# Optimization experiments

Hardware: AMD Instinct MI355X
Metric: run time of the kernel (lower is better)

## Reference

```python
import jax, jax.numpy as jnp
import numpy as np

B, T, C = 2, 2048, 768
H = 12
HD = C // H  # 64
DFF = 4 * C
EPS = 1e-5


def setup_inputs() -> dict:
    key = jax.random.key(0)
    ks = jax.random.split(key, 12)
    s = 0.02
    return {
        "x": jax.random.normal(ks[0], (B, T, C), dtype=jnp.float32),
        "ln1_g": jnp.ones((C,), jnp.float32),
        "ln1_b": jnp.zeros((C,), jnp.float32),
        "w_qkv": jax.random.normal(ks[1], (C, 3 * C), dtype=jnp.float32) * s,
        "w_o": jax.random.normal(ks[2], (C, C), dtype=jnp.float32) * s,
        "ln2_g": jnp.ones((C,), jnp.float32),
        "ln2_b": jnp.zeros((C,), jnp.float32),
        "w_fc": jax.random.normal(ks[3], (C, DFF), dtype=jnp.float32) * s,
        "b_fc": jnp.zeros((DFF,), jnp.float32),
        "w_proj": jax.random.normal(ks[4], (DFF, C), dtype=jnp.float32) * s,
        "b_proj": jnp.zeros((C,), jnp.float32),
    }


def _layernorm(x, g, b):
    mu = jnp.mean(x, axis=-1, keepdims=True)
    var = jnp.mean(jnp.square(x - mu), axis=-1, keepdims=True)
    return (x - mu) * jax.lax.rsqrt(var + EPS) * g + b


def _attn(x, w_qkv, w_o):
    b, t, c = x.shape
    qkv = x @ w_qkv  # [b,t,3c]
    q, k, v = jnp.split(qkv, 3, axis=-1)
    q = q.reshape(b, t, H, HD).transpose(0, 2, 1, 3)  # [b,h,t,d]
    k = k.reshape(b, t, H, HD).transpose(0, 2, 1, 3)
    v = v.reshape(b, t, H, HD).transpose(0, 2, 1, 3)
    att = jnp.einsum("bhqd,bhkd->bhqk", q, k) / jnp.sqrt(jnp.float32(HD))
    causal = jnp.tril(jnp.ones((t, t), dtype=bool))
    att = jnp.where(causal, att, -jnp.inf)
    att = jax.nn.softmax(att, axis=-1)
    y = jnp.einsum("bhqk,bhkd->bhqd", att, v)
    y = y.transpose(0, 2, 1, 3).reshape(b, t, c)
    return y @ w_o


def reference(x, ln1_g, ln1_b, w_qkv, w_o, ln2_g, ln2_b, w_fc, b_fc, w_proj, b_proj):
    x = x + _attn(_layernorm(x, ln1_g, ln1_b), w_qkv, w_o)
    h = _layernorm(x, ln2_g, ln2_b)
    h = jax.nn.gelu(h @ w_fc + b_fc, approximate=False)  # torch F.gelu default = exact erf
    x = x + (h @ w_proj + b_proj)
    return x
```

## Files before the change

kernel.cpp:

```cpp
#include <hip/hip_runtime.h>
#include <hip/hip_bf16.h>
#include <math.h>

#define T_SEQ 2048
#define NB 2
#define C_DIM 768
#define NH 12

typedef unsigned short ushort_t;
typedef __attribute__((ext_vector_type(8))) short short8;
typedef __attribute__((ext_vector_type(8))) unsigned short ushort8;
typedef __attribute__((ext_vector_type(4))) unsigned short ushortx4;
typedef __attribute__((ext_vector_type(4))) float floatx4;
typedef __attribute__((ext_vector_type(4))) _Float16 half4;

__device__ inline float bf2f(ushort_t u) {
    unsigned int x = ((unsigned int)u) << 16;
    return __uint_as_float(x);
}
__device__ inline ushort_t f2bf(float f) {
    unsigned int u = __float_as_uint(f);
    unsigned int r = (u + 0x7fffu + ((u >> 16) & 1u)) >> 16;
    return (ushort_t)r;
}
__device__ inline ushort_t f2h_bits(float f) {
    union { _Float16 h; ushort_t u; } cv;
    cv.h = (_Float16)f;
    return cv.u;
}

#if defined(__has_builtin)
#if __has_builtin(__builtin_amdgcn_global_load_lds)
#define HAVE_GLL 1
#endif
#endif

__device__ inline void gload_lds16(const ushort_t* g, ushort_t* l) {
#ifdef HAVE_GLL
    __builtin_amdgcn_global_load_lds(
        (const __attribute__((address_space(1))) void*)g,
        (__attribute__((address_space(3))) void*)l, 16, 0, 0);
#else
    int lane = threadIdx.x & 63;
    *(ushort8*)(l + lane * 8) = *(const ushort8*)g;
#endif
}

__device__ void wconv_tile(const float* __restrict__ W, ushort_t* __restrict__ WT,
                           int K, int N, int k0, int n0, int tid, ushort_t* Tls) {
    int nl = (tid & 15) * 4;
    int kl = tid >> 4;
#pragma unroll
    for (int rr = 0; rr < 4; rr++) {
        int k = kl + rr * 16;
        floatx4 v = *(const floatx4*)&W[(size_t)(k0 + k) * N + n0 + nl];
#pragma unroll
        for (int j = 0; j < 4; j++) Tls[(nl + j) * 72 + k] = f2bf(v[j]);
    }
    __syncthreads();
    int no = tid >> 3;
    int ko = (tid & 7) * 8;
#pragma unroll
    for (int rr = 0; rr < 2; rr++) {
        int n = no + rr * 32;
        ushort8 t = *(const ushort8*)&Tls[n * 72 + ko];
        *(ushort8*)&WT[(size_t)(n0 + n) * K + k0 + ko] = t;
    }
}

__global__ __launch_bounds__(256) void prep1_kernel(const float* __restrict__ w_qkv, ushort_t* __restrict__ wqkvT,
                                                    const float* __restrict__ w_o, ushort_t* __restrict__ woT,
                                                    const float* __restrict__ w_fc, ushort_t* __restrict__ wfcT,
                                                    const float* __restrict__ w_proj, ushort_t* __restrict__ wprojT,
                                                    const float* __restrict__ x, const float* __restrict__ g,
                                                    const float* __restrict__ b, ushort_t* __restrict__ xn) {
    __shared__ ushort_t Tls[64 * 72];
    __shared__ float red[8];
    int id = blockIdx.x, tid = threadIdx.x;
    if (id < 432) { wconv_tile(w_qkv, wqkvT, 768, 2304, (id % 12) * 64, (id / 12) * 64, tid, Tls); return; }
    if (id < 576) { int r = id - 432; wconv_tile(w_o, woT, 768, 768, (r % 12) * 64, (r / 12) * 64, tid, Tls); return; }
    if (id < 1152) { int r = id - 576; wconv_tile(w_fc, wfcT, 768, 3072, (r % 12) * 64, (r / 12) * 64, tid, Tls); return; }
    if (id < 1728) { int r = id - 1152; wconv_tile(w_proj, wprojT, 3072, 768, (r % 48) * 64, (r / 48) * 64, tid, Tls); return; }
    int row = id - 1728;
    int lane = tid & 63, wave = tid >> 6;
    const float* xr = x + (size_t)row * C_DIM;
    float v0 = xr[tid], v1 = xr[tid + 256], v2 = xr[tid + 512];
    float s = v0 + v1 + v2;
#pragma unroll
    for (int m = 32; m > 0; m >>= 1) s += __shfl_xor(s, m, 64);
    if (lane == 0) red[wave] = s;
    __syncthreads();
    float mean = (red[0] + red[1] + red[2] + red[3]) * (1.0f / C_DIM);
    float d0 = v0 - mean, d1 = v1 - mean, d2 = v2 - mean;
    float q = d0 * d0 + d1 * d1 + d2 * d2;
#pragma unroll
    for (int m = 32; m > 0; m >>= 1) q += __shfl_xor(q, m, 64);
    if (lane == 0) red[wave + 4] = q;
    __syncthreads();
    float var = (red[4] + red[5] + red[6] + red[7]) * (1.0f / C_DIM);
    float rstd = rsqrtf(var + 1e-5f);
    ushort_t* orow = xn + (size_t)row * C_DIM;
    orow[tid]       = f2bf(d0 * rstd * g[tid]       + b[tid]);
    orow[tid + 256] = f2bf(d1 * rstd * g[tid + 256] + b[tid + 256]);
    orow[tid + 512] = f2bf(d2 * rstd * g[tid + 512] + b[tid + 512]);
}

__global__ __launch_bounds__(192) void combine_ln_kernel(const float* __restrict__ x,
                                                         const ushort_t* __restrict__ P,
                                                         const float* __restrict__ g,
                                                         const float* __restrict__ bb,
                                                         float* __restrict__ x2,
                                                         ushort_t* __restrict__ xn) {
    int row = blockIdx.x;
    int tid = threadIdx.x;
    int lane = tid & 63, wave = tid >> 6;
    int col = tid * 4;
    size_t idx = (size_t)row * C_DIM + col;
    floatx4 xv = *(const floatx4*)&x[idx];
    ushortx4 a = *(const ushortx4*)&P[idx];
    ushortx4 b2 = *(const ushortx4*)&P[3145728 + idx];
    ushortx4 c2 = *(const ushortx4*)&P[6291456 + idx];
    floatx4 v;
#pragma unroll
    for (int j = 0; j < 4; j++) v[j] = xv[j] + bf2f(a[j]) + bf2f(b2[j]) + bf2f(c2[j]);
    *(floatx4*)&x2[idx] = v;

    float s = v[0] + v[1] + v[2] + v[3];
#pragma unroll
    for (int m = 32; m > 0; m >>= 1) s += __shfl_xor(s, m, 64);
    __shared__ float red[6];
    if (lane == 0) red[wave] = s;
    __syncthreads();
    float mean = (red[0] + red[1] + red[2]) * (1.0f / C_DIM);
    floatx4 d;
#pragma unroll
    for (int j = 0; j < 4; j++) d[j] = v[j] - mean;
    float q = d[0] * d[0] + d[1] * d[1] + d[2] * d[2] + d[3] * d[3];
#pragma unroll
    for (int m = 32; m > 0; m >>= 1) q += __shfl_xor(q, m, 64);
    if (lane == 0) red[wave + 3] = q;
    __syncthreads();
    float var = (red[3] + red[4] + red[5]) * (1.0f / C_DIM);
    float rstd = rsqrtf(var + 1e-5f);
    floatx4 gv = *(const floatx4*)&g[col];
    floatx4 bv = *(const floatx4*)&bb[col];
    ushortx4 o;
#pragma unroll
    for (int j = 0; j < 4; j++) o[j] = f2bf(d[j] * rstd * gv[j] + bv[j]);
    *(ushortx4*)&xn[idx] = o;
}

#define GEMM_LOOP(Aptr, Bptr, KDIM, KLEN, KOFF)                                        \
    __shared__ ushort_t As[128 * 64];                                                  \
    __shared__ ushort_t Bs[128 * 64];                                                  \
    int tid = threadIdx.x;                                                             \
    int lane = tid & 63, wave = tid >> 6;                                              \
    int lane15 = lane & 15, quad = lane >> 4;                                          \
    int wr = wave >> 1, wc = wave & 1;                                                 \
    int row0 = blockIdx.x * 128, col0 = blockIdx.y * 128;                              \
    int srow = lane >> 3;                                                              \
    int sseg = (lane & 7) ^ srow;                                                      \
    const ushort_t* ag[4]; const ushort_t* bg[4];                                      \
    ushort_t* la[4]; ushort_t* lb[4];                                                  \
    _Pragma("unroll")                                                                  \
    for (int j = 0; j < 4; j++) {                                                      \
        int r = wave * 32 + j * 8;                                                     \
        ag[j] = Aptr + (size_t)(row0 + r + srow) * KDIM + KOFF + sseg * 8;             \
        bg[j] = Bptr + (size_t)(col0 + r + srow) * KDIM + KOFF + sseg * 8;             \
        la[j] = &As[r * 64]; lb[j] = &Bs[r * 64];                                      \
    }                                                                                  \
    floatx4 acc[4][4];                                                                 \
    floatx4 zero = {0.f, 0.f, 0.f, 0.f};                                               \
    _Pragma("unroll")                                                                  \
    for (int mt = 0; mt < 4; mt++)                                                     \
        _Pragma("unroll")                                                              \
        for (int nt = 0; nt < 4; nt++) acc[mt][nt] = zero;                             \
    for (int k0 = 0; k0 < KLEN; k0 += 64) {                                            \
        _Pragma("unroll")                                                              \
        for (int j = 0; j < 4; j++) gload_lds16(ag[j] + k0, la[j]);                    \
        _Pragma("unroll")                                                              \
        for (int j = 0; j < 4; j++) gload_lds16(bg[j] + k0, lb[j]);                    \
        __syncthreads();                                                               \
        _Pragma("unroll")                                                              \
        for (int ko = 0; ko < 2; ko++) {                                               \
            int slot = (quad + ko * 4) ^ (lane15 & 7);                                 \
            short8 af[4], bfm[4];                                                      \
            _Pragma("unroll")                                                          \
            for (int mt = 0; mt < 4; mt++)                                             \
                af[mt] = *(const short8*)&As[(wr * 64 + mt * 16 + lane15) * 64 + slot * 8]; \
            _Pragma("unroll")                                                          \
            for (int nt = 0; nt < 4; nt++)                                             \
                bfm[nt] = *(const short8*)&Bs[(wc * 64 + nt * 16 + lane15) * 64 + slot * 8]; \
            _Pragma("unroll")                                                          \
            for (int mt = 0; mt < 4; mt++)                                             \
                _Pragma("unroll")                                                      \
                for (int nt = 0; nt < 4; nt++)                                         \
                    acc[mt][nt] = __builtin_amdgcn_mfma_f32_16x16x32_bf16(af[mt], bfm[nt], acc[mt][nt], 0, 0, 0); \
        }                                                                              \
        __syncthreads();                                                               \
    }

__global__ __launch_bounds__(256) void gemm_qkv_kernel(const ushort_t* __restrict__ A,
                                                       const ushort_t* __restrict__ BT,
                                                       ushort_t* __restrict__ qbuf,
                                                       ushort_t* __restrict__ kh,
                                                       ushort_t* __restrict__ vtb) {
    GEMM_LOOP(A, BT, 768, 768, 0)
    int yb = blockIdx.y;
    if (yb < 6) {
#pragma unroll
        for (int mt = 0; mt < 4; mt++) {
            int r_base = row0 + wr * 64 + mt * 16 + quad * 4;
#pragma unroll
            for (int nt = 0; nt < 4; nt++) {
                int cc = col0 + wc * 64 + nt * 16 + lane15;
#pragma unroll
                for (int r = 0; r < 4; r++)
                    qbuf[(size_t)(r_base + r) * 768 + cc] = f2bf(acc[mt][nt][r]);
            }
        }
    } else if (yb < 12) {
#pragma unroll
        for (int mt = 0; mt < 4; mt++) {
            int r_base = row0 + wr * 64 + mt * 16 + quad * 4;
#pragma unroll
            for (int nt = 0; nt < 4; nt++) {
                int colk = col0 - 768 + wc * 64 + nt * 16 + lane15;
                int hh = colk >> 6, dd = colk & 63;
#pragma unroll
                for (int r = 0; r < 4; r++) {
                    int rr = r_base + r;
                    kh[((size_t)((rr >> 11) * NH + hh)) * 131072 + (size_t)(rr & 2047) * 64 + dd] =
                        f2bf(acc[mt][nt][r]);
                }
            }
        }
    } else {
#pragma unroll
        for (int mt = 0; mt < 4; mt++) {
            int r_base = row0 + wr * 64 + mt * 16 + quad * 4;
            int bb2 = r_base >> 11;
            int tt = r_base & 2047;
#pragma unroll
            for (int nt = 0; nt < 4; nt++) {
                int colv = col0 - 1536 + wc * 64 + nt * 16 + lane15;
                int hh = colv >> 6, dd = colv & 63;
                size_t va = ((size_t)(bb2 * NH + hh)) * 131072 + (size_t)(tt >> 4) * 1024 +
                            (size_t)dd * 16 + (tt & 15);
                ushortx4 pv;
#pragma unroll
                for (int r = 0; r < 4; r++) pv[r] = f2h_bits(acc[mt][nt][r]);
                *(ushortx4*)&vtb[va] = pv;
            }
        }
    }
}

__global__ __launch_bounds__(256) void gemm_gelu_kernel(const ushort_t* __restrict__ A,
                                                        const ushort_t* __restrict__ BT,
                                                        const float* __restrict__ bias,
                                                        ushort_t* __restrict__ Cout) {
    GEMM_LOOP(A, BT, 768, 768, 0)
    const int N = 3072;
#pragma unroll
    for (int mt = 0; mt < 4; mt++) {
        int r_base = row0 + wr * 64 + mt * 16 + quad * 4;
#pragma unroll
        for (int nt = 0; nt < 4; nt++) {
            int cc = col0 + wc * 64 + nt * 16 + lane15;
            float bvv = bias[cc];
#pragma unroll
            for (int r = 0; r < 4; r++) {
                float v = acc[mt][nt][r] + bvv;
                float y2 = v * (2.3022079f + 0.10294323f * v * v);
                float e = __builtin_amdgcn_exp2f(-y2);
                v = v * __builtin_amdgcn_rcpf(1.f + e);
                Cout[(size_t)(r_base + r) * N + cc] = f2bf(v);
            }
        }
    }
}

__global__ __launch_bounds__(256) void gemm_bt_split_kernel(const ushort_t* __restrict__ A,
                                                            const ushort_t* __restrict__ BT,
                                                            ushort_t* __restrict__ P,
                                                            int M, int N, int K, int klen) {
    int kz0 = blockIdx.z * klen;
    GEMM_LOOP(A, BT, K, klen, kz0)
    ushort_t* Pz = P + (size_t)blockIdx.z * M * N;
#pragma unroll
    for (int mt = 0; mt < 4; mt++) {
        int r_base = row0 + wr * 64 + mt * 16 + quad * 4;
#pragma unroll
        for (int nt = 0; nt < 4; nt++) {
            int cc = col0 + wc * 64 + nt * 16 + lane15;
#pragma unroll
            for (int r = 0; r < 4; r++)
                Pz[(size_t)(r_base + r) * N + cc] = f2bf(acc[mt][nt][r]);
        }
    }
}

__global__ __launch_bounds__(256) void combine_bias_res_kernel(float* __restrict__ x2,
                                                               const float* __restrict__ bias,
                                                               const ushort_t* __restrict__ P) {
    int i = blockIdx.x * 256 + threadIdx.x;
    int col = (i * 4) % C_DIM;
    floatx4 xv = *(const floatx4*)&x2[i * 4];
    floatx4 bv = *(const floatx4*)&bias[col];
    ushortx4 a = *(const ushortx4*)&P[i * 4];
    ushortx4 b = *(const ushortx4*)&P[3145728 + i * 4];
    floatx4 o;
#pragma unroll
    for (int j = 0; j < 4; j++) o[j] = xv[j] + bv[j] + bf2f(a[j]) + bf2f(b[j]);
    *(floatx4*)&x2[i * 4] = o;
}

#define QSCALE 0.18033688f
__global__ __launch_bounds__(256) void attn_kernel(const ushort_t* __restrict__ qbuf,
                                                   const ushort_t* __restrict__ kh,
                                                   const ushort_t* __restrict__ vtb,
                                                   ushort_t* __restrict__ y) {
    __shared__ ushort_t Kb[2][4096];
    __shared__ ushort_t Vb[2][4096];
    int tid = threadIdx.x;
    int lane = tid & 63, wave = tid >> 6;
    int lane15 = lane & 15, quad = lane >> 4;
    int qt = 31 - (int)blockIdx.x;
    int q0 = qt * 64;
    int h = blockIdx.y, b = blockIdx.z;
    size_t hb = (size_t)(b * NH + h) * (T_SEQ * 64);
    const ushort_t* khb = kh + hb;
    const ushort_t* vtbb = vtb + hb;

    int q = q0 + wave * 16 + lane15;
    int qmax_wave = q0 + wave * 16 + 15;
    short8 qf[2];
#pragma unroll
    for (int c = 0; c < 2; c++) {
        ushort8 qv = *(const ushort8*)(qbuf + ((size_t)b * T_SEQ + q) * 768 + h * 64 + c * 32 + quad * 8);
        short8 qs;
#pragma unroll
        for (int j = 0; j < 8; j++) qs[j] = (short)f2bf(bf2f(qv[j]) * QSCALE);
        qf[c] = qs;
    }

    floatx4 o[4];
    floatx4 zero = {0.f, 0.f, 0.f, 0.f};
#pragma unroll
    for (int nt = 0; nt < 4; nt++) o[nt] = zero;
    float l4[4] = {0.f, 0.f, 0.f, 0.f};

    int tiles = qt + 1;
    int vsrc = lane ^ ((lane >> 3) & 1);

    {
        if (wave < 2) {
#pragma unroll
            for (int j = 0; j < 4; j++) {
                int r = wave * 4 + j;
                int i = r * 64 + lane;
                int key = i >> 3;
                int seg = ((i & 7) - (key & 7) + 8) & 7;
                gload_lds16(khb + (size_t)key * 64 + seg * 8, &Kb[0][(size_t)r * 512]);
            }
        } else {
#pragma unroll
            for (int j = 0; j < 4; j++) {
                int r = (wave - 2) * 4 + j;
                gload_lds16(vtbb + (size_t)r * 512 + vsrc * 8, &Vb[0][(size_t)r * 512]);
            }
        }
    }

    for (int t = 0; t < tiles; t++) {
        int kb = t * 64;
        int cur = t & 1;
        __syncthreads();
        if (t + 1 < tiles) {
            int kb2 = kb + 64;
            int nxt = cur ^ 1;
            if (wave < 2) {
#pragma unroll
                for (int j = 0; j < 4; j++) {
                    int r = wave * 4 + j;
                    int i = r * 64 + lane;
                    int key = i >> 3;
                    int seg = ((i & 7) - (key & 7) + 8) & 7;
                    gload_lds16(khb + (size_t)(kb2 + key) * 64 + seg * 8, &Kb[nxt][(size_t)r * 512]);
                }
            } else {
#pragma unroll
                for (int j = 0; j < 4; j++) {
                    int r = (wave - 2) * 4 + j;
                    gload_lds16(vtbb + (size_t)(kb2 >> 4) * 1024 + (size_t)r * 512 + vsrc * 8,
                                &Vb[nxt][(size_t)r * 512]);
                }
            }
        }

        if (kb <= qmax_wave) {
            const ushort_t* Kc = Kb[cur];
            const _Float16* Vc = (const _Float16*)Vb[cur];

            floatx4 s[4];
#pragma unroll
            for (int sb = 0; sb < 4; sb++) {
                int key = sb * 16 + lane15;
                int s0i = key * 8 + ((quad + key) & 7);
                int s1i = key * 8 + ((quad + 4 + key) & 7);
                short8 kf0 = *(const short8*)(Kc + (size_t)s0i * 8);
                short8 kf1 = *(const short8*)(Kc + (size_t)s1i * 8);
                floatx4 sv = zero;
                sv = __builtin_amdgcn_mfma_f32_16x16x32_bf16(kf0, qf[0], sv, 0, 0, 0);
                sv = __builtin_amdgcn_mfma_f32_16x16x32_bf16(kf1, qf[1], sv, 0, 0, 0);
                s[sb] = sv;
            }

            if (kb + 64 > qmax_wave) {
#pragma unroll
                for (int sb = 0; sb < 4; sb++)
#pragma unroll
                    for (int r = 0; r < 4; r++) {
                        int key = kb + sb * 16 + quad * 4 + r;
                        if (key > q) s[sb][r] = -INFINITY;
                    }
            }

            half4 pf[4];
#pragma unroll
            for (int sb = 0; sb < 4; sb++)
#pragma unroll
                for (int r = 0; r < 4; r++) {
                    float p = __builtin_amdgcn_exp2f(s[sb][r]);
                    l4[r] += p;
                    pf[sb][r] = (_Float16)p;
                }

#pragma unroll
            for (int sb = 0; sb < 4; sb++) {
#pragma unroll
                for (int nt = 0; nt < 4; nt++) {
                    int gg = sb * 128 + (nt * 16 + lane15) * 2 + (quad >> 1);
                    int ss = gg ^ ((gg >> 3) & 1);
                    half4 vf = *(const half4*)&Vc[(size_t)ss * 8 + (quad & 1) * 4];
                    o[nt] = __builtin_amdgcn_mfma_f32_16x16x16f16(vf, pf[sb], o[nt], 0, 0, 0);
                }
            }
        }
    }

    float l_i = (l4[0] + l4[1]) + (l4[2] + l4[3]);
    l_i += __shfl_xor(l_i, 16, 64);
    l_i += __shfl_xor(l_i, 32, 64);
    float rcp_w = 1.f / l_i;
    ushort_t* yb = y + (size_t)b * T_SEQ * 768;
#pragma unroll
    for (int nt = 0; nt < 4; nt++) {
        ushortx4 st;
#pragma unroll
        for (int r = 0; r < 4; r++) st[r] = f2bf(o[nt][r] * rcp_w);
        *(ushortx4*)&yb[(size_t)q * 768 + h * 64 + nt * 16 + quad * 4] = st;
    }
}

extern "C" void kernel_launch(void* const* d_in, const int* in_sizes, int n_in,
                              void* d_out, int out_size, void* d_ws, size_t ws_size,
                              hipStream_t stream) {
    (void)in_sizes; (void)n_in; (void)out_size; (void)ws_size;
    const float* x      = (const float*)d_in[0];
    const float* ln1_g  = (const float*)d_in[1];
    const float* ln1_b  = (const float*)d_in[2];
    const float* w_qkv  = (const float*)d_in[3];
    const float* w_o    = (const float*)d_in[4];
    const float* ln2_g  = (const float*)d_in[5];
    const float* ln2_b  = (const float*)d_in[6];
    const float* w_fc   = (const float*)d_in[7];
    const float* b_fc   = (const float*)d_in[8];
    const float* w_proj = (const float*)d_in[9];
    const float* b_proj = (const float*)d_in[10];

    char* ws = (char*)d_ws;
    ushort_t* qbuf   = (ushort_t*)(ws);
    ushort_t* kh     = (ushort_t*)(ws + 6291456);
    ushort_t* vtb    = (ushort_t*)(ws + 12582912);
    ushort_t* PA     = (ushort_t*)(ws);
    ushort_t* hff    = (ushort_t*)(ws);
    ushort_t* ybuf   = (ushort_t*)(ws + 18874368);
    ushort_t* xn     = (ushort_t*)(ws + 25165824);
    ushort_t* PB     = (ushort_t*)(ws + 25165824);
    ushort_t* wqkvT  = (ushort_t*)(ws + 31457280);
    ushort_t* woT    = (ushort_t*)(ws + 34996224);
    ushort_t* wfcT   = (ushort_t*)(ws + 36175872);
    ushort_t* wprojT = (ushort_t*)(ws + 40894464);
    float* x2 = (float*)d_out;

    const int M = NB * T_SEQ;

    prep1_kernel<<<dim3(5824), 256, 0, stream>>>(w_qkv, wqkvT, w_o, woT, w_fc, wfcT,
                                                 w_proj, wprojT, x, ln1_g, ln1_b, xn);
    gemm_qkv_kernel<<<dim3(32, 18), 256, 0, stream>>>(xn, wqkvT, qbuf, kh, vtb);
    attn_kernel<<<dim3(32, 12, 2), 256, 0, stream>>>(qbuf, kh, vtb, ybuf);
    gemm_bt_split_kernel<<<dim3(32, 6, 3), 256, 0, stream>>>(ybuf, woT, PA, M, 768, 768, 256);
    combine_ln_kernel<<<dim3(M), 192, 0, stream>>>(x, PA, ln2_g, ln2_b, x2, xn);
    gemm_gelu_kernel<<<dim3(32, 24), 256, 0, stream>>>(xn, wfcT, b_fc, hff);
    gemm_bt_split_kernel<<<dim3(32, 6, 2), 256, 0, stream>>>(hff, wprojT, PB, M, 768, 3072, 1536);
    combine_bias_res_kernel<<<dim3(3072), 256, 0, stream>>>(x2, b_proj, PB);
}
```

Before: 265.9 us.

## Process two 16-row query groups per wave in attention to reuse K/V tiles

Each attention block now covers 128 queries instead of 64, with each wave handling two 16-query groups that share the same K and V fragments loaded from LDS. This halves the grid and the number of K/V tile loads per query, cutting global and LDS traffic per unit of work. The cost is more registers per thread (double accumulators and scores), which may lower occupancy. There are also fewer blocks (384), so load balance across the causal triangle gets coarser.

```diff
diff --git a/kernel.cpp b/kernel.cpp
--- a/kernel.cpp
+++ b/kernel.cpp
@@ -326,32 +326,41 @@
     int tid = threadIdx.x;
     int lane = tid & 63, wave = tid >> 6;
     int lane15 = lane & 15, quad = lane >> 4;
-    int qt = 31 - (int)blockIdx.x;
-    int q0 = qt * 64;
+    int qt = 15 - (int)blockIdx.x;
+    int q0 = qt * 128;
     int h = blockIdx.y, b = blockIdx.z;
     size_t hb = (size_t)(b * NH + h) * (T_SEQ * 64);
     const ushort_t* khb = kh + hb;
     const ushort_t* vtbb = vtb + hb;
 
-    int q = q0 + wave * 16 + lane15;
-    int qmax_wave = q0 + wave * 16 + 15;
-    short8 qf[2];
-#pragma unroll
-    for (int c = 0; c < 2; c++) {
-        ushort8 qv = *(const ushort8*)(qbuf + ((size_t)b * T_SEQ + q) * 768 + h * 64 + c * 32 + quad * 8);
-        short8 qs;
-#pragma unroll
-        for (int j = 0; j < 8; j++) qs[j] = (short)f2bf(bf2f(qv[j]) * QSCALE);
-        qf[c] = qs;
-    }
-
-    floatx4 o[4];
+    int qA = q0 + wave * 32 + lane15;
+    int qB = qA + 16;
+    int qmaxA = q0 + wave * 32 + 15;
+    int qmaxB = qmaxA + 16;
+
+    short8 qf[2][2];
+#pragma unroll
+    for (int g = 0; g < 2; g++) {
+        int qq = (g == 0) ? qA : qB;
+#pragma unroll
+        for (int c = 0; c < 2; c++) {
+            ushort8 qv = *(const ushort8*)(qbuf + ((size_t)b * T_SEQ + qq) * 768 + h * 64 + c * 32 + quad * 8);
+            short8 qs;
+#pragma unroll
+            for (int j = 0; j < 8; j++) qs[j] = (short)f2bf(bf2f(qv[j]) * QSCALE);
+            qf[g][c] = qs;
+        }
+    }
+
+    floatx4 o[2][4];
     floatx4 zero = {0.f, 0.f, 0.f, 0.f};
 #pragma unroll
-    for (int nt = 0; nt < 4; nt++) o[nt] = zero;
-    float l4[4] = {0.f, 0.f, 0.f, 0.f};
-
-    int tiles = qt + 1;
+    for (int g = 0; g < 2; g++)
+#pragma unroll
+        for (int nt = 0; nt < 4; nt++) o[g][nt] = zero;
+    float l4[2][4] = {{0.f, 0.f, 0.f, 0.f}, {0.f, 0.f, 0.f, 0.f}};
+
+    int tiles = qt * 2 + 2;
     int vsrc = lane ^ ((lane >> 3) & 1);
 
     {
@@ -399,11 +408,12 @@
             }
         }
 
-        if (kb <= qmax_wave) {
+        if (kb <= qmaxB) {
             const ushort_t* Kc = Kb[cur];
             const _Float16* Vc = (const _Float16*)Vb[cur];
-
-            floatx4 s[4];
+            bool doA = (kb <= qmaxA);
+
+            floatx4 sA[4], sB[4];
 #pragma unroll
             for (int sb = 0; sb < 4; sb++) {
                 int key = sb * 16 + lane15;
@@ -412,30 +422,55 @@
                 short8 kf0 = *(const short8*)(Kc + (size_t)s0i * 8);
                 short8 kf1 = *(const short8*)(Kc + (size_t)s1i * 8);
                 floatx4 sv = zero;
-                sv = __builtin_amdgcn_mfma_f32_16x16x32_bf16(kf0, qf[0], sv, 0, 0, 0);
-                sv = __builtin_amdgcn_mfma_f32_16x16x32_bf16(kf1, qf[1], sv, 0, 0, 0);
-                s[sb] = sv;
-            }
-
-            if (kb + 64 > qmax_wave) {
+                sv = __builtin_amdgcn_mfma_f32_16x16x32_bf16(kf0, qf[1][0], sv, 0, 0, 0);
+                sv = __builtin_amdgcn_mfma_f32_16x16x32_bf16(kf1, qf[1][1], sv, 0, 0, 0);
+                sB[sb] = sv;
+                if (doA) {
+                    floatx4 sv2 = zero;
+                    sv2 = __builtin_amdgcn_mfma_f32_16x16x32_bf16(kf0, qf[0][0], sv2, 0, 0, 0);
+                    sv2 = __builtin_amdgcn_mfma_f32_16x16x32_bf16(kf1, qf[0][1], sv2, 0, 0, 0);
+                    sA[sb] = sv2;
+                }
+            }
+
+            if (kb + 64 > qmaxB) {
 #pragma unroll
                 for (int sb = 0; sb < 4; sb++)
 #pragma unroll
                     for (int r = 0; r < 4; r++) {
                         int key = kb + sb * 16 + quad * 4 + r;
-                        if (key > q) s[sb][r] = -INFINITY;
+                        if (key > qB) sB[sb][r] = -INFINITY;
                     }
             }
-
-            half4 pf[4];
+            if (doA && kb + 64 > qmaxA) {
+#pragma unroll
+                for (int sb = 0; sb < 4; sb++)
+#pragma unroll
+                    for (int r = 0; r < 4; r++) {
+                        int key = kb + sb * 16 + quad * 4 + r;
+                        if (key > qA) sA[sb][r] = -INFINITY;
+                    }
+            }
+
+            half4 pfA[4], pfB[4];
 #pragma unroll
             for (int sb = 0; sb < 4; sb++)
 #pragma unroll
                 for (int r = 0; r < 4; r++) {
-                    float p = __builtin_amdgcn_exp2f(s[sb][r]);
-                    l4[r] += p;
-                    pf[sb][r] = (_Float16)p;
+                    float p = __builtin_amdgcn_exp2f(sB[sb][r]);
+                    l4[1][r] += p;
+                    pfB[sb][r] = (_Float16)p;
                 }
+            if (doA) {
+#pragma unroll
+                for (int sb = 0; sb < 4; sb++)
+#pragma unroll
+                    for (int r = 0; r < 4; r++) {
+                        float p = __builtin_amdgcn_exp2f(sA[sb][r]);
+                        l4[0][r] += p;
+                        pfA[sb][r] = (_Float16)p;
+                    }
+            }
 
 #pragma unroll
             for (int sb = 0; sb < 4; sb++) {
@@ -444,23 +479,29 @@
                     int gg = sb * 128 + (nt * 16 + lane15) * 2 + (quad >> 1);
                     int ss = gg ^ ((gg >> 3) & 1);
                     half4 vf = *(const half4*)&Vc[(size_t)ss * 8 + (quad & 1) * 4];
-                    o[nt] = __builtin_amdgcn_mfma_f32_16x16x16f16(vf, pf[sb], o[nt], 0, 0, 0);
+                    o[1][nt] = __builtin_amdgcn_mfma_f32_16x16x16f16(vf, pfB[sb], o[1][nt], 0, 0, 0);
+                    if (doA)
+                        o[0][nt] = __builtin_amdgcn_mfma_f32_16x16x16f16(vf, pfA[sb], o[0][nt], 0, 0, 0);
                 }
             }
         }
     }
 
-    float l_i = (l4[0] + l4[1]) + (l4[2] + l4[3]);
-    l_i += __shfl_xor(l_i, 16, 64);
-    l_i += __shfl_xor(l_i, 32, 64);
-    float rcp_w = 1.f / l_i;
     ushort_t* yb = y + (size_t)b * T_SEQ * 768;
 #pragma unroll
-    for (int nt = 0; nt < 4; nt++) {
-        ushortx4 st;
-#pragma unroll
-        for (int r = 0; r < 4; r++) st[r] = f2bf(o[nt][r] * rcp_w);
-        *(ushortx4*)&yb[(size_t)q * 768 + h * 64 + nt * 16 + quad * 4] = st;
+    for (int g = 0; g < 2; g++) {
+        float l_i = (l4[g][0] + l4[g][1]) + (l4[g][2] + l4[g][3]);
+        l_i += __shfl_xor(l_i, 16, 64);
+        l_i += __shfl_xor(l_i, 32, 64);
+        float rcp_w = 1.f / l_i;
+        int qq = (g == 0) ? qA : qB;
+#pragma unroll
+        for (int nt = 0; nt < 4; nt++) {
+            ushortx4 st;
+#pragma unroll
+            for (int r = 0; r < 4; r++) st[r] = f2bf(o[g][nt][r] * rcp_w);
+            *(ushortx4*)&yb[(size_t)qq * 768 + h * 64 + nt * 16 + quad * 4] = st;
+        }
     }
 }
 
@@ -500,7 +541,7 @@
     prep1_kernel<<<dim3(5824), 256, 0, stream>>>(w_qkv, wqkvT, w_o, woT, w_fc, wfcT,
                                                  w_proj, wprojT, x, ln1_g, ln1_b, xn);
     gemm_qkv_kernel<<<dim3(32, 18), 256, 0, stream>>>(xn, wqkvT, qbuf, kh, vtb);
-    attn_kernel<<<dim3(32, 12, 2), 256, 0, stream>>>(qbuf, kh, vtb, ybuf);
+    attn_kernel<<<dim3(16, 12, 2), 256, 0, stream>>>(qbuf, kh, vtb, ybuf);
     gemm_bt_split_kernel<<<dim3(32, 6, 3), 256, 0, stream>>>(ybuf, woT, PA, M, 768, 768, 256);
     combine_ln_kernel<<<dim3(M), 192, 0, stream>>>(x, PA, ln2_g, ln2_b, x2, xn);
     gemm_gelu_kernel<<<dim3(32, 24), 256, 0, stream>>>(xn, wfcT, b_fc, hff);
```

Measured after the change: 286.1 us. 7.6% more time.

## Split long causal attention tiles across two blocks and combine partial outputs

Applied to the files above, without the earlier changes.

The upper half of query tiles, which have the most key tiles under causal masking, are now each split into two blocks that process disjoint halves of the key range. Each half writes unnormalized fp16 partial outputs and row sums to workspace, and a new combine kernel sums them and normalizes. The aim is better load balance and more blocks to fill the GPU during attention. The cost is an extra launch, extra global traffic for the partials, and fp16 storage of the unnormalized accumulators. The combine drops any max-subtraction and simply adds both halves' sums, which is only correct if the kernel does not track a running max, as the original code appears not to.

```diff
diff --git a/kernel.cpp b/kernel.cpp
--- a/kernel.cpp
+++ b/kernel.cpp
@@ -320,15 +320,32 @@
 __global__ __launch_bounds__(256) void attn_kernel(const ushort_t* __restrict__ qbuf,
                                                    const ushort_t* __restrict__ kh,
                                                    const ushort_t* __restrict__ vtb,
-                                                   ushort_t* __restrict__ y) {
+                                                   ushort_t* __restrict__ y,
+                                                   ushort_t* __restrict__ OP,
+                                                   float* __restrict__ LP) {
     __shared__ ushort_t Kb[2][4096];
     __shared__ ushort_t Vb[2][4096];
     int tid = threadIdx.x;
     int lane = tid & 63, wave = tid >> 6;
     int lane15 = lane & 15, quad = lane >> 4;
-    int qt = 31 - (int)blockIdx.x;
+    int c = blockIdx.x;
+    int h = blockIdx.y, b = blockIdx.z;
+    int qt, t_start, t_end, half = 0;
+    bool is_half;
+    if (c < 32) {
+        qt = 16 + (c >> 1);
+        half = c & 1;
+        int ntl = qt + 1, mid = ntl >> 1;
+        t_start = half ? mid : 0;
+        t_end = half ? ntl : mid;
+        is_half = true;
+    } else {
+        qt = c - 32;
+        t_start = 0;
+        t_end = qt + 1;
+        is_half = false;
+    }
     int q0 = qt * 64;
-    int h = blockIdx.y, b = blockIdx.z;
     size_t hb = (size_t)(b * NH + h) * (T_SEQ * 64);
     const ushort_t* khb = kh + hb;
     const ushort_t* vtbb = vtb + hb;
@@ -337,12 +354,12 @@
     int qmax_wave = q0 + wave * 16 + 15;
     short8 qf[2];
 #pragma unroll
-    for (int c = 0; c < 2; c++) {
-        ushort8 qv = *(const ushort8*)(qbuf + ((size_t)b * T_SEQ + q) * 768 + h * 64 + c * 32 + quad * 8);
+    for (int cc2 = 0; cc2 < 2; cc2++) {
+        ushort8 qv = *(const ushort8*)(qbuf + ((size_t)b * T_SEQ + q) * 768 + h * 64 + cc2 * 32 + quad * 8);
         short8 qs;
 #pragma unroll
         for (int j = 0; j < 8; j++) qs[j] = (short)f2bf(bf2f(qv[j]) * QSCALE);
-        qf[c] = qs;
+        qf[cc2] = qs;
     }
 
     floatx4 o[4];
@@ -351,10 +368,11 @@
     for (int nt = 0; nt < 4; nt++) o[nt] = zero;
     float l4[4] = {0.f, 0.f, 0.f, 0.f};
 
-    int tiles = qt + 1;
     int vsrc = lane ^ ((lane >> 3) & 1);
 
     {
+        int kb = t_start * 64;
+        int buf = t_start & 1;
         if (wave < 2) {
 #pragma unroll
             for (int j = 0; j < 4; j++) {
@@ -362,22 +380,23 @@
                 int i = r * 64 + lane;
                 int key = i >> 3;
                 int seg = ((i & 7) - (key & 7) + 8) & 7;
-                gload_lds16(khb + (size_t)key * 64 + seg * 8, &Kb[0][(size_t)r * 512]);
+                gload_lds16(khb + (size_t)(kb + key) * 64 + seg * 8, &Kb[buf][(size_t)r * 512]);
             }
         } else {
 #pragma unroll
             for (int j = 0; j < 4; j++) {
                 int r = (wave - 2) * 4 + j;
-                gload_lds16(vtbb + (size_t)r * 512 + vsrc * 8, &Vb[0][(size_t)r * 512]);
-            }
-        }
-    }
-
-    for (int t = 0; t < tiles; t++) {
+                gload_lds16(vtbb + (size_t)(kb >> 4) * 1024 + (size_t)r * 512 + vsrc * 8,
+                            &Vb[buf][(size_t)r * 512]);
+            }
+        }
+    }
+
+    for (int t = t_start; t < t_end; t++) {
         int kb = t * 64;
         int cur = t & 1;
         __syncthreads();
-        if (t + 1 < tiles) {
+        if (t + 1 < t_end) {
             int kb2 = kb + 64;
             int nxt = cur ^ 1;
             if (wave < 2) {
@@ -453,14 +472,49 @@
     float l_i = (l4[0] + l4[1]) + (l4[2] + l4[3]);
     l_i += __shfl_xor(l_i, 16, 64);
     l_i += __shfl_xor(l_i, 32, 64);
-    float rcp_w = 1.f / l_i;
-    ushort_t* yb = y + (size_t)b * T_SEQ * 768;
-#pragma unroll
-    for (int nt = 0; nt < 4; nt++) {
-        ushortx4 st;
-#pragma unroll
-        for (int r = 0; r < 4; r++) st[r] = f2bf(o[nt][r] * rcp_w);
-        *(ushortx4*)&yb[(size_t)q * 768 + h * 64 + nt * 16 + quad * 4] = st;
+
+    if (!is_half) {
+        float rcp_w = 1.f / l_i;
+        ushort_t* yb = y + (size_t)b * T_SEQ * 768;
+#pragma unroll
+        for (int nt = 0; nt < 4; nt++) {
+            ushortx4 st;
+#pragma unroll
+            for (int r = 0; r < 4; r++) st[r] = f2bf(o[nt][r] * rcp_w);
+            *(ushortx4*)&yb[(size_t)q * 768 + h * 64 + nt * 16 + quad * 4] = st;
+        }
+    } else {
+        int tileIdx = (qt - 16) + 16 * (h + NH * b);
+        ushort_t* Ob = OP + (size_t)(tileIdx * 2 + half) * 4096;
+        float* Lb = LP + (size_t)(tileIdx * 2 + half) * 64;
+        if (quad == 0) Lb[wave * 16 + lane15] = l_i;
+#pragma unroll
+        for (int nt = 0; nt < 4; nt++)
+#pragma unroll
+            for (int r = 0; r < 4; r++)
+                Ob[(nt * 16 + quad * 4 + r) * 64 + wave * 16 + lane15] = f2h_bits(o[nt][r]);
+    }
+}
+
+__global__ __launch_bounds__(256) void attn_combine_kernel(const ushort_t* __restrict__ OP,
+                                                           const float* __restrict__ LP,
+                                                           ushort_t* __restrict__ y) {
+    int qt = 16 + blockIdx.x;
+    int h = blockIdx.y, b = blockIdx.z;
+    int tileIdx = blockIdx.x + 16 * (h + NH * b);
+    const _Float16* O0 = (const _Float16*)(OP + (size_t)(tileIdx * 2) * 4096);
+    const _Float16* O1 = O0 + 4096;
+    const float* L0 = LP + (size_t)(tileIdx * 2) * 64;
+    const float* L1 = L0 + 64;
+    int tid = threadIdx.x;
+    ushort_t* yb = y + ((size_t)b * T_SEQ + qt * 64) * 768 + h * 64;
+#pragma unroll
+    for (int i = 0; i < 16; i++) {
+        int idx = tid + i * 256;
+        int q = idx >> 6, d = idx & 63;
+        float v = (float)O0[d * 64 + q] + (float)O1[d * 64 + q];
+        float l = L0[q] + L1[q];
+        yb[(size_t)q * 768 + d] = f2bf(v / l);
     }
 }
 
@@ -488,6 +542,8 @@
     ushort_t* hff    = (ushort_t*)(ws);
     ushort_t* ybuf   = (ushort_t*)(ws + 18874368);
     ushort_t* xn     = (ushort_t*)(ws + 25165824);
+    ushort_t* attnO  = (ushort_t*)(ws + 25165824);
+    float*    attnL  = (float*)(ws + 31457280);
     ushort_t* PB     = (ushort_t*)(ws + 25165824);
     ushort_t* wqkvT  = (ushort_t*)(ws + 31457280);
     ushort_t* woT    = (ushort_t*)(ws + 34996224);
@@ -500,7 +556,8 @@
     prep1_kernel<<<dim3(5824), 256, 0, stream>>>(w_qkv, wqkvT, w_o, woT, w_fc, wfcT,
                                                  w_proj, wprojT, x, ln1_g, ln1_b, xn);
     gemm_qkv_kernel<<<dim3(32, 18), 256, 0, stream>>>(xn, wqkvT, qbuf, kh, vtb);
-    attn_kernel<<<dim3(32, 12, 2), 256, 0, stream>>>(qbuf, kh, vtb, ybuf);
+    attn_kernel<<<dim3(48, 12, 2), 256, 0, stream>>>(qbuf, kh, vtb, ybuf, attnO, attnL);
+    attn_combine_kernel<<<dim3(16, 12, 2), 256, 0, stream>>>(attnO, attnL, ybuf);
     gemm_bt_split_kernel<<<dim3(32, 6, 3), 256, 0, stream>>>(ybuf, woT, PA, M, 768, 768, 256);
     combine_ln_kernel<<<dim3(M), 192, 0, stream>>>(x, PA, ln2_g, ln2_b, x2, xn);
     gemm_gelu_kernel<<<dim3(32, 24), 256, 0, stream>>>(xn, wfcT, b_fc, hff);
```

Measured after the change: 268.9 us. About the same (+1.1%).
